# Optimization experiments

Hardware: AMD Instinct MI355X
Metric: run time of the kernel (lower is better)

Reference implementation:

```python
import jax, jax.numpy as jnp
import numpy as np

N = 100_000          # number of nodes
E = 3_200_000        # number of edges (avg degree 32)
IN_CH = 128
OUT_CH = 128


def setup_inputs() -> dict:
    key = jax.random.key(0)
    k1, k2, k3, k4 = jax.random.split(key, 4)
    x = jax.random.normal(k1, (N, IN_CH), dtype=jnp.float32)
    edge_index = jax.random.randint(k2, (2, E), 0, N, dtype=jnp.int32)
    # torch nn.Linear weights have shape [out_features, in_features]
    W_theta = jax.random.normal(k3, (OUT_CH, IN_CH), dtype=jnp.float32) / np.sqrt(IN_CH).astype(np.float32)
    W_phi = jax.random.normal(k4, (OUT_CH, OUT_CH), dtype=jnp.float32) / np.sqrt(OUT_CH).astype(np.float32)
    return {"x": x, "edge_index": edge_index, "W_theta": W_theta, "W_phi": W_phi}


def reference(x, edge_index, W_theta, W_phi):
    row, col = edge_index[0], edge_index[1]
    rel_pos = x[row] - x[col]                       # [E, in]
    rel_t = rel_pos @ W_theta.T                     # [E, out]
    aggr = jax.ops.segment_max(rel_t, row, num_segments=N)  # [N, out], -inf for empty segments
    # torch_scatter.scatter_max leaves empty segments at 0
    aggr = jnp.where(jnp.isneginf(aggr), jnp.zeros((), dtype=aggr.dtype), aggr)
    return aggr @ W_phi.T                           # [N, out]
```

## Files before the change

kernel.cpp:

```cpp
#include <hip/hip_runtime.h>
#include <stdint.h>

#define N_NODES 100000
#define N_EDGES 3200000
#define CH 128
#define NBUK 391
#define CAP 8704
#define SPLITB 391
#define EPB 8192
#define ROWS_A 50048

typedef __bf16 bf16x8 __attribute__((ext_vector_type(8)));
typedef float  floatx4 __attribute__((ext_vector_type(4)));

__device__ __forceinline__ unsigned short f2bf_bits(float f) {
    unsigned u = __float_as_uint(f);
    u += 0x7FFFu + ((u >> 16) & 1u);
    return (unsigned short)(u >> 16);
}

__device__ __forceinline__ unsigned short enc16(unsigned short b) {
    return b ^ ((b & 0x8000u) ? 0xFFFFu : 0x8000u);
}

__device__ __forceinline__ unsigned pkminu(unsigned a, unsigned b) {
    unsigned d;
    asm("v_pk_min_u16 %0, %1, %2" : "=v"(d) : "v"(a), "v"(b));
    return d;
}

__device__ __forceinline__ unsigned dec2(unsigned k) {
    unsigned lo = k & 0xFFFFu;
    unsigned hi = k >> 16;
    lo ^= (lo & 0x8000u) ? 0x8000u : 0xFFFFu;
    hi ^= (hi & 0x8000u) ? 0x8000u : 0xFFFFu;
    return lo | (hi << 16);
}

__device__ __forceinline__ bf16x8 pack8(floatx4 f0, floatx4 f1) {
    bf16x8 r;
    r[0] = (__bf16)f0[0]; r[1] = (__bf16)f0[1]; r[2] = (__bf16)f0[2]; r[3] = (__bf16)f0[3];
    r[4] = (__bf16)f1[0]; r[5] = (__bf16)f1[1]; r[6] = (__bf16)f1[2]; r[7] = (__bf16)f1[3];
    return r;
}

__device__ __forceinline__ void gemm_tile(int row0, int lane, const float* __restrict__ x,
                                          const unsigned short* __restrict__ wb,
                                          unsigned short* __restrict__ yt) {
    int m = lane & 15, quad = lane >> 4;
    bf16x8 a[4];
    const floatx4* xp = (const floatx4*)(x + (size_t)(row0 + m) * CH + quad * 8);
#pragma unroll
    for (int ks = 0; ks < 4; ks++) a[ks] = pack8(xp[ks * 8], xp[ks * 8 + 1]);

    for (int nt = 0; nt < 8; nt++) {
        const bf16x8* wp = (const bf16x8*)(wb + (size_t)(nt * 16 + m) * CH + quad * 8);
        floatx4 acc = {0.f, 0.f, 0.f, 0.f};
#pragma unroll
        for (int ks = 0; ks < 4; ks++)
            acc = __builtin_amdgcn_mfma_f32_16x16x32_bf16(a[ks], wp[ks * 4], acc, 0, 0, 0);
#pragma unroll
        for (int r = 0; r < 4; r++) {
            int orow = row0 + quad * 4 + r;
            yt[(size_t)orow * CH + nt * 16 + m] = enc16(f2bf_bits(acc[r]));
        }
    }
}

__global__ void k_setup(const float* __restrict__ Wt, const float* __restrict__ Wp,
                        unsigned short* __restrict__ wb, int* __restrict__ cursor) {
    int bid = blockIdx.x, t = threadIdx.x;
    if (bid < 128) {
        int i = bid * 256 + t;
        float v = (i < 16384) ? Wt[i] : Wp[i - 16384];
        wb[i] = f2bf_bits(v);
    } else {
        for (int i = t; i < NBUK; i += 256) cursor[i] = i * CAP;
    }
}

__global__ void k_split_gemmyA(const int* __restrict__ row, const int* __restrict__ col,
                               int* __restrict__ cursor, unsigned* __restrict__ pairs,
                               const float* __restrict__ x,
                               const unsigned short* __restrict__ wb,
                               unsigned short* __restrict__ yt) {
    __shared__ unsigned lpair[EPB];
    __shared__ int h[NBUK];
    __shared__ int hb[NBUK];
    __shared__ int lbase[NBUK];
    __shared__ int cur[NBUK];
    __shared__ int sc[512];
    int bid = blockIdx.x, t = threadIdx.x;
    if (bid < SPLITB) {
        for (int i = t; i < NBUK; i += 256) h[i] = 0;
        __syncthreads();
        int e0 = bid * EPB;
        int4 r[8];
        bool v[8];
#pragma unroll
        for (int j = 0; j < 8; j++) {
            int idx = e0 + j * 1024 + t * 4;
            v[j] = idx < N_EDGES;
            if (v[j]) {
                r[j] = *(const int4*)(row + idx);
                atomicAdd(&h[r[j].x >> 8], 1);
                atomicAdd(&h[r[j].y >> 8], 1);
                atomicAdd(&h[r[j].z >> 8], 1);
                atomicAdd(&h[r[j].w >> 8], 1);
            }
        }
        __syncthreads();
        for (int i = t; i < NBUK; i += 256) {
            int c = h[i];
            hb[i] = c ? atomicAdd(&cursor[i], c) : 0;
        }
        sc[t] = h[t];
        sc[t + 256] = (t + 256 < NBUK) ? h[t + 256] : 0;
        __syncthreads();
        for (int off = 1; off < 512; off <<= 1) {
            int a0 = (t >= off) ? sc[t - off] : 0;
            int a1 = (t + 256 >= off) ? sc[t + 256 - off] : 0;
            __syncthreads();
            sc[t] += a0;
            sc[t + 256] += a1;
            __syncthreads();
        }
        for (int i = t; i < NBUK; i += 256) {
            int lb = sc[i] - h[i];
            lbase[i] = lb;
            cur[i] = lb;
        }
        __syncthreads();
#pragma unroll
        for (int j = 0; j < 8; j++) {
            if (v[j]) {
                int idx = e0 + j * 1024 + t * 4;
                int4 c = *(const int4*)(col + idx);
                int b, p;
                b = r[j].x >> 8; p = atomicAdd(&cur[b], 1);
                lpair[p] = ((unsigned)(r[j].x & 255) << 17) | (unsigned)c.x;
                b = r[j].y >> 8; p = atomicAdd(&cur[b], 1);
                lpair[p] = ((unsigned)(r[j].y & 255) << 17) | (unsigned)c.y;
                b = r[j].z >> 8; p = atomicAdd(&cur[b], 1);
                lpair[p] = ((unsigned)(r[j].z & 255) << 17) | (unsigned)c.z;
                b = r[j].w >> 8; p = atomicAdd(&cur[b], 1);
                lpair[p] = ((unsigned)(r[j].w & 255) << 17) | (unsigned)c.w;
            }
        }
        __syncthreads();
        for (int b = t; b < NBUK; b += 256) {
            int n = h[b];
            if (!n) continue;
            int src = lbase[b];
            int dst = hb[b];
            int lim = (b + 1) * CAP - dst;
            if (n > lim) n = lim;
            for (int k = 0; k < n; k++) pairs[dst + k] = lpair[src + k];
        }
    } else {
        int wave = (bid - SPLITB) * 4 + (t >> 6);
        int row0 = wave * 16;
        if (row0 >= ROWS_A) return;
        gemm_tile(row0, t & 63, x, wb, yt);
    }
}

__global__ void k_build_gemmyB(unsigned* __restrict__ pairs, const int* __restrict__ cursor,
                               int* __restrict__ deg, int* __restrict__ offs,
                               const float* __restrict__ x,
                               const unsigned short* __restrict__ wb,
                               unsigned short* __restrict__ yt) {
    __shared__ int hist[256];
    __shared__ int sc[256];
    __shared__ int cur[256];
    __shared__ int lcsr[CAP];
    int bid = blockIdx.x, t = threadIdx.x;
    if (bid < NBUK) {
        int b = bid;
        int s0 = b * CAP;
        int cnt = cursor[b] - s0;
        if (cnt > CAP) cnt = CAP;
        if (t < 256) hist[t] = 0;
        __syncthreads();
        for (int i = t; i < cnt; i += 1024) {
            unsigned p = pairs[s0 + i];
            atomicAdd(&hist[p >> 17], 1);
        }
        __syncthreads();
        int d = 0;
        if (t < 256) { d = hist[t]; sc[t] = d; }
        __syncthreads();
        for (int off = 1; off < 256; off <<= 1) {
            int vv = 0;
            if (t < 256 && t >= off) vv = sc[t - off];
            __syncthreads();
            if (t < 256) sc[t] += vv;
            __syncthreads();
        }
        if (t < 256) {
            int excl = sc[t] - d;
            int node = b * 256 + t;
            if (node < N_NODES) {
                deg[node] = d;
                offs[node] = s0 + excl;
            }
            cur[t] = excl;
        }
        __syncthreads();
        for (int i = t; i < cnt; i += 1024) {
            unsigned p = pairs[s0 + i];
            int pos = atomicAdd(&cur[p >> 17], 1);
            lcsr[pos] = (int)(p & 0x1FFFFu);
        }
        __syncthreads();
        int* csr = (int*)pairs;
        for (int i = t; i < cnt; i += 1024) csr[s0 + i] = lcsr[i];
    } else {
        int wg = (bid - NBUK) * 16 + (t >> 6);
        int row0 = ROWS_A + wg * 16;
        if (row0 >= N_NODES) return;
        gemm_tile(row0, t & 63, x, wb, yt);
    }
}

#define PKA(v)                        \
    do {                              \
        m0 = pkminu(m0, (v).x);       \
        m1 = pkminu(m1, (v).y);       \
        m2 = pkminu(m2, (v).z);       \
        m3 = pkminu(m3, (v).w);       \
    } while (0)

__global__ void k_minaggr_out(const uint4* __restrict__ yt, const int* __restrict__ offs,
                              const int* __restrict__ deg, const int* __restrict__ csr,
                              const unsigned short* __restrict__ wb,
                              float* __restrict__ out) {
    __shared__ unsigned short atile[16 * 136];
    int t = threadIdx.x;
    int wave = t >> 6, lane = t & 63;
    int q = lane >> 4, s = lane & 15;
    int nl = wave * 4 + q;
    int n = blockIdx.x * 16 + nl;

    int i = offs[n];
    int len = deg[n];
    int end = i + len;

    unsigned m0 = ~0u, m1 = ~0u, m2 = ~0u, m3 = ~0u;

    for (; i + 8 <= end; i += 8) {
        int c0 = csr[i + 0];
        int c1 = csr[i + 1];
        int c2 = csr[i + 2];
        int c3 = csr[i + 3];
        int c4 = csr[i + 4];
        int c5 = csr[i + 5];
        int c6 = csr[i + 6];
        int c7 = csr[i + 7];
        uint4 v0 = yt[(size_t)c0 * 16 + s];
        uint4 v1 = yt[(size_t)c1 * 16 + s];
        uint4 v2 = yt[(size_t)c2 * 16 + s];
        uint4 v3 = yt[(size_t)c3 * 16 + s];
        uint4 v4 = yt[(size_t)c4 * 16 + s];
        uint4 v5 = yt[(size_t)c5 * 16 + s];
        uint4 v6 = yt[(size_t)c6 * 16 + s];
        uint4 v7 = yt[(size_t)c7 * 16 + s];
        PKA(v0); PKA(v1); PKA(v2); PKA(v3);
        PKA(v4); PKA(v5); PKA(v6); PKA(v7);
    }
    for (; i < end; i++) {
        int c = csr[i];
        uint4 v = yt[(size_t)c * 16 + s];
        PKA(v);
    }

    uint4 outv = {0u, 0u, 0u, 0u};
    if (len > 0) {
        unsigned d0 = dec2(m0), d1 = dec2(m1), d2 = dec2(m2), d3 = dec2(m3);
        uint4 se = yt[(size_t)n * 16 + s];
        unsigned s0 = dec2(se.x), s1 = dec2(se.y), s2 = dec2(se.z), s3 = dec2(se.w);
        outv.x = (unsigned)f2bf_bits(__uint_as_float(s0 << 16) - __uint_as_float(d0 << 16)) |
                 ((unsigned)f2bf_bits(__uint_as_float(s0 & 0xFFFF0000u) -
                                      __uint_as_float(d0 & 0xFFFF0000u)) << 16);
        outv.y = (unsigned)f2bf_bits(__uint_as_float(s1 << 16) - __uint_as_float(d1 << 16)) |
                 ((unsigned)f2bf_bits(__uint_as_float(s1 & 0xFFFF0000u) -
                                      __uint_as_float(d1 & 0xFFFF0000u)) << 16);
        outv.z = (unsigned)f2bf_bits(__uint_as_float(s2 << 16) - __uint_as_float(d2 << 16)) |
                 ((unsigned)f2bf_bits(__uint_as_float(s2 & 0xFFFF0000u) -
                                      __uint_as_float(d2 & 0xFFFF0000u)) << 16);
        outv.w = (unsigned)f2bf_bits(__uint_as_float(s3 << 16) - __uint_as_float(d3 << 16)) |
                 ((unsigned)f2bf_bits(__uint_as_float(s3 & 0xFFFF0000u) -
                                      __uint_as_float(d3 & 0xFFFF0000u)) << 16);
    }
    *(uint4*)&atile[nl * 136 + s * 8] = outv;
    __syncthreads();

    int m = lane & 15, quad = lane >> 4;
    bf16x8 a[4];
#pragma unroll
    for (int ks = 0; ks < 4; ks++)
        a[ks] = *(const bf16x8*)&atile[m * 136 + ks * 32 + quad * 8];

#pragma unroll
    for (int ntl = 0; ntl < 2; ntl++) {
        int nt = wave * 2 + ntl;
        const bf16x8* wp = (const bf16x8*)(wb + (size_t)(nt * 16 + m) * CH + quad * 8);
        floatx4 acc = {0.f, 0.f, 0.f, 0.f};
#pragma unroll
        for (int ks = 0; ks < 4; ks++)
            acc = __builtin_amdgcn_mfma_f32_16x16x32_bf16(a[ks], wp[ks * 4], acc, 0, 0, 0);
#pragma unroll
        for (int r = 0; r < 4; r++)
            out[(size_t)(blockIdx.x * 16 + quad * 4 + r) * CH + nt * 16 + m] = acc[r];
    }
}

extern "C" void kernel_launch(void* const* d_in, const int* in_sizes, int n_in,
                              void* d_out, int out_size, void* d_ws, size_t ws_size,
                              hipStream_t stream) {
    const float* x   = (const float*)d_in[0];
    const int* edge  = (const int*)d_in[1];
    const float* Wt  = (const float*)d_in[2];
    const float* Wp  = (const float*)d_in[3];
    const int* row = edge;
    const int* col = edge + N_EDGES;
    float* out = (float*)d_out;

    char* ws = (char*)d_ws;
    int* deg    = (int*)ws;  ws += 400128;
    int* offs   = (int*)ws;  ws += 400128;
    int* cursor = (int*)ws;  ws += 2048;
    unsigned short* yt = (unsigned short*)ws; ws += 25600000;
    unsigned short* wb = (unsigned short*)ws; ws += 65536;
    unsigned* pairs = (unsigned*)ws; ws += (size_t)NBUK * CAP * 4;

    k_setup<<<129, 256, 0, stream>>>(Wt, Wp, wb, cursor);
    k_split_gemmyA<<<SPLITB + 782, 256, 0, stream>>>(row, col, cursor, pairs, x, wb, yt);
    k_build_gemmyB<<<NBUK + 196, 1024, 0, stream>>>(pairs, cursor, deg, offs, x, wb, yt);
    k_minaggr_out<<<N_NODES / 16, 256, 0, stream>>>((const uint4*)yt, offs, deg,
                                                    (const int*)pairs, wb + 16384, out);
}
```

Baseline: 278.2 us.

## Fuse CSR build into min-aggregation kernel and move all node GEMM to split kernel

Removes the separate build kernel. Each bucket is now processed by two 512-thread blocks, one per half of the bucket's 256 nodes. Each block re-reads the bucket's pairs, builds a local CSR in shared memory, runs the packed-min gather over yt, and performs the output GEMM for its 128 nodes. The first-stage GEMM for all nodes moves into the split kernel, which drops one launch and the global CSR, deg and offs round trips. The cost is that every bucket's pairs are read twice, fewer and larger blocks run the gather, and each block holds more shared memory, which may reduce occupancy and latency hiding.

```diff
diff --git a/kernel.cpp b/kernel.cpp
--- a/kernel.cpp
+++ b/kernel.cpp
@@ -8,7 +8,6 @@
 #define CAP 8704
 #define SPLITB 391
 #define EPB 8192
-#define ROWS_A 50048
 
 typedef __bf16 bf16x8 __attribute__((ext_vector_type(8)));
 typedef float  floatx4 __attribute__((ext_vector_type(4)));
@@ -42,6 +41,26 @@
     r[0] = (__bf16)f0[0]; r[1] = (__bf16)f0[1]; r[2] = (__bf16)f0[2]; r[3] = (__bf16)f0[3];
     r[4] = (__bf16)f1[0]; r[5] = (__bf16)f1[1]; r[6] = (__bf16)f1[2]; r[7] = (__bf16)f1[3];
     return r;
+}
+
+__device__ __forceinline__ uint4 finish_half(unsigned m0, unsigned m1, unsigned m2, unsigned m3,
+                                             uint4 se) {
+    unsigned d0 = dec2(m0), d1 = dec2(m1), d2 = dec2(m2), d3 = dec2(m3);
+    unsigned s0 = dec2(se.x), s1 = dec2(se.y), s2 = dec2(se.z), s3 = dec2(se.w);
+    uint4 o;
+    o.x = (unsigned)f2bf_bits(__uint_as_float(s0 << 16) - __uint_as_float(d0 << 16)) |
+          ((unsigned)f2bf_bits(__uint_as_float(s0 & 0xFFFF0000u) -
+                               __uint_as_float(d0 & 0xFFFF0000u)) << 16);
+    o.y = (unsigned)f2bf_bits(__uint_as_float(s1 << 16) - __uint_as_float(d1 << 16)) |
+          ((unsigned)f2bf_bits(__uint_as_float(s1 & 0xFFFF0000u) -
+                               __uint_as_float(d1 & 0xFFFF0000u)) << 16);
+    o.z = (unsigned)f2bf_bits(__uint_as_float(s2 << 16) - __uint_as_float(d2 << 16)) |
+          ((unsigned)f2bf_bits(__uint_as_float(s2 & 0xFFFF0000u) -
+                               __uint_as_float(d2 & 0xFFFF0000u)) << 16);
+    o.w = (unsigned)f2bf_bits(__uint_as_float(s3 << 16) - __uint_as_float(d3 << 16)) |
+          ((unsigned)f2bf_bits(__uint_as_float(s3 & 0xFFFF0000u) -
+                               __uint_as_float(d3 & 0xFFFF0000u)) << 16);
+    return o;
 }
 
 __device__ __forceinline__ void gemm_tile(int row0, int lane, const float* __restrict__ x,
@@ -79,7 +98,7 @@
     }
 }
 
-__global__ void k_split_gemmyA(const int* __restrict__ row, const int* __restrict__ col,
+__global__ void k_split_gemmyF(const int* __restrict__ row, const int* __restrict__ col,
                                int* __restrict__ cursor, unsigned* __restrict__ pairs,
                                const float* __restrict__ x,
                                const unsigned short* __restrict__ wb,
@@ -160,158 +179,132 @@
     } else {
         int wave = (bid - SPLITB) * 4 + (t >> 6);
         int row0 = wave * 16;
-        if (row0 >= ROWS_A) return;
-        gemm_tile(row0, t & 63, x, wb, yt);
-    }
-}
-
-__global__ void k_build_gemmyB(unsigned* __restrict__ pairs, const int* __restrict__ cursor,
-                               int* __restrict__ deg, int* __restrict__ offs,
-                               const float* __restrict__ x,
-                               const unsigned short* __restrict__ wb,
-                               unsigned short* __restrict__ yt) {
-    __shared__ int hist[256];
-    __shared__ int sc[256];
-    __shared__ int cur[256];
-    __shared__ int lcsr[CAP];
-    int bid = blockIdx.x, t = threadIdx.x;
-    if (bid < NBUK) {
-        int b = bid;
-        int s0 = b * CAP;
-        int cnt = cursor[b] - s0;
-        if (cnt > CAP) cnt = CAP;
-        if (t < 256) hist[t] = 0;
-        __syncthreads();
-        for (int i = t; i < cnt; i += 1024) {
-            unsigned p = pairs[s0 + i];
-            atomicAdd(&hist[p >> 17], 1);
-        }
-        __syncthreads();
-        int d = 0;
-        if (t < 256) { d = hist[t]; sc[t] = d; }
-        __syncthreads();
-        for (int off = 1; off < 256; off <<= 1) {
-            int vv = 0;
-            if (t < 256 && t >= off) vv = sc[t - off];
-            __syncthreads();
-            if (t < 256) sc[t] += vv;
-            __syncthreads();
-        }
-        if (t < 256) {
-            int excl = sc[t] - d;
-            int node = b * 256 + t;
-            if (node < N_NODES) {
-                deg[node] = d;
-                offs[node] = s0 + excl;
-            }
-            cur[t] = excl;
-        }
-        __syncthreads();
-        for (int i = t; i < cnt; i += 1024) {
-            unsigned p = pairs[s0 + i];
-            int pos = atomicAdd(&cur[p >> 17], 1);
-            lcsr[pos] = (int)(p & 0x1FFFFu);
-        }
-        __syncthreads();
-        int* csr = (int*)pairs;
-        for (int i = t; i < cnt; i += 1024) csr[s0 + i] = lcsr[i];
-    } else {
-        int wg = (bid - NBUK) * 16 + (t >> 6);
-        int row0 = ROWS_A + wg * 16;
         if (row0 >= N_NODES) return;
         gemm_tile(row0, t & 63, x, wb, yt);
     }
 }
 
-#define PKA(v)                        \
+#define PK4(M, v)                     \
     do {                              \
-        m0 = pkminu(m0, (v).x);       \
-        m1 = pkminu(m1, (v).y);       \
-        m2 = pkminu(m2, (v).z);       \
-        m3 = pkminu(m3, (v).w);       \
+        (M).x = pkminu((M).x, (v).x); \
+        (M).y = pkminu((M).y, (v).y); \
+        (M).z = pkminu((M).z, (v).z); \
+        (M).w = pkminu((M).w, (v).w); \
     } while (0)
 
-__global__ void k_minaggr_out(const uint4* __restrict__ yt, const int* __restrict__ offs,
-                              const int* __restrict__ deg, const int* __restrict__ csr,
-                              const unsigned short* __restrict__ wb,
-                              float* __restrict__ out) {
-    __shared__ unsigned short atile[16 * 136];
+__global__ __launch_bounds__(512) void k_buildmin_out(
+        const unsigned* __restrict__ pairs, const int* __restrict__ cursor,
+        const uint4* __restrict__ yt, const unsigned short* __restrict__ wb,
+        float* __restrict__ out) {
+    __shared__ int hist[128];
+    __shared__ int scn[128];
+    __shared__ int basep[128];
+    __shared__ int curn[128];
+    __shared__ char ubuf[CAP * 4];
+    int* lcsr = (int*)ubuf;
+    unsigned short* atile = (unsigned short*)ubuf;
+
     int t = threadIdx.x;
+    int b = blockIdx.x >> 1;
+    int half = blockIdx.x & 1;
+    int s0 = b * CAP;
+    int cnt = cursor[b] - s0;
+    if (cnt > CAP) cnt = CAP;
+
+    if (t < 128) hist[t] = 0;
+    __syncthreads();
+    for (int i = t; i < cnt; i += 512) {
+        unsigned p = pairs[s0 + i];
+        int local = (int)(p >> 17);
+        if ((local >> 7) == half) atomicAdd(&hist[local & 127], 1);
+    }
+    __syncthreads();
+    int d = 0;
+    if (t < 128) { d = hist[t]; scn[t] = d; }
+    __syncthreads();
+    for (int off = 1; off < 128; off <<= 1) {
+        int vv = 0;
+        if (t < 128 && t >= off) vv = scn[t - off];
+        __syncthreads();
+        if (t < 128) scn[t] += vv;
+        __syncthreads();
+    }
+    if (t < 128) {
+        int excl = scn[t] - d;
+        basep[t] = excl;
+        curn[t] = excl;
+    }
+    __syncthreads();
+    for (int i = t; i < cnt; i += 512) {
+        unsigned p = pairs[s0 + i];
+        int local = (int)(p >> 17);
+        if ((local >> 7) == half) {
+            int pos = atomicAdd(&curn[local & 127], 1);
+            lcsr[pos] = (int)(p & 0x1FFFFu);
+        }
+    }
+    __syncthreads();
+
+    int s16 = t & 15;
+    int nsub = t >> 4;
+    uint4 sv[4];
+#pragma unroll
+    for (int ng = 0; ng < 4; ng++) {
+        int l = ng * 32 + nsub;
+        int i = basep[l];
+        int len = hist[l];
+        int end = i + len;
+        uint4 M = {~0u, ~0u, ~0u, ~0u};
+        for (; i + 8 <= end; i += 8) {
+            int c0 = lcsr[i + 0], c1 = lcsr[i + 1], c2 = lcsr[i + 2], c3 = lcsr[i + 3];
+            int c4 = lcsr[i + 4], c5 = lcsr[i + 5], c6 = lcsr[i + 6], c7 = lcsr[i + 7];
+            uint4 v0 = yt[(size_t)c0 * 16 + s16];
+            uint4 v1 = yt[(size_t)c1 * 16 + s16];
+            uint4 v2 = yt[(size_t)c2 * 16 + s16];
+            uint4 v3 = yt[(size_t)c3 * 16 + s16];
+            uint4 v4 = yt[(size_t)c4 * 16 + s16];
+            uint4 v5 = yt[(size_t)c5 * 16 + s16];
+            uint4 v6 = yt[(size_t)c6 * 16 + s16];
+            uint4 v7 = yt[(size_t)c7 * 16 + s16];
+            PK4(M, v0); PK4(M, v1); PK4(M, v2); PK4(M, v3);
+            PK4(M, v4); PK4(M, v5); PK4(M, v6); PK4(M, v7);
+        }
+        for (; i < end; i++) {
+            uint4 v = yt[(size_t)lcsr[i] * 16 + s16];
+            PK4(M, v);
+        }
+        uint4 outv = {0u, 0u, 0u, 0u};
+        if (len > 0) {
+            int n = blockIdx.x * 128 + l;
+            outv = finish_half(M.x, M.y, M.z, M.w, yt[(size_t)n * 16 + s16]);
+        }
+        sv[ng] = outv;
+    }
+    __syncthreads();
+#pragma unroll
+    for (int ng = 0; ng < 4; ng++)
+        *(uint4*)&atile[(ng * 32 + nsub) * 136 + s16 * 8] = sv[ng];
+    __syncthreads();
+
     int wave = t >> 6, lane = t & 63;
-    int q = lane >> 4, s = lane & 15;
-    int nl = wave * 4 + q;
-    int n = blockIdx.x * 16 + nl;
-
-    int i = offs[n];
-    int len = deg[n];
-    int end = i + len;
-
-    unsigned m0 = ~0u, m1 = ~0u, m2 = ~0u, m3 = ~0u;
-
-    for (; i + 8 <= end; i += 8) {
-        int c0 = csr[i + 0];
-        int c1 = csr[i + 1];
-        int c2 = csr[i + 2];
-        int c3 = csr[i + 3];
-        int c4 = csr[i + 4];
-        int c5 = csr[i + 5];
-        int c6 = csr[i + 6];
-        int c7 = csr[i + 7];
-        uint4 v0 = yt[(size_t)c0 * 16 + s];
-        uint4 v1 = yt[(size_t)c1 * 16 + s];
-        uint4 v2 = yt[(size_t)c2 * 16 + s];
-        uint4 v3 = yt[(size_t)c3 * 16 + s];
-        uint4 v4 = yt[(size_t)c4 * 16 + s];
-        uint4 v5 = yt[(size_t)c5 * 16 + s];
-        uint4 v6 = yt[(size_t)c6 * 16 + s];
-        uint4 v7 = yt[(size_t)c7 * 16 + s];
-        PKA(v0); PKA(v1); PKA(v2); PKA(v3);
-        PKA(v4); PKA(v5); PKA(v6); PKA(v7);
-    }
-    for (; i < end; i++) {
-        int c = csr[i];
-        uint4 v = yt[(size_t)c * 16 + s];
-        PKA(v);
-    }
-
-    uint4 outv = {0u, 0u, 0u, 0u};
-    if (len > 0) {
-        unsigned d0 = dec2(m0), d1 = dec2(m1), d2 = dec2(m2), d3 = dec2(m3);
-        uint4 se = yt[(size_t)n * 16 + s];
-        unsigned s0 = dec2(se.x), s1 = dec2(se.y), s2 = dec2(se.z), s3 = dec2(se.w);
-        outv.x = (unsigned)f2bf_bits(__uint_as_float(s0 << 16) - __uint_as_float(d0 << 16)) |
-                 ((unsigned)f2bf_bits(__uint_as_float(s0 & 0xFFFF0000u) -
-                                      __uint_as_float(d0 & 0xFFFF0000u)) << 16);
-        outv.y = (unsigned)f2bf_bits(__uint_as_float(s1 << 16) - __uint_as_float(d1 << 16)) |
-                 ((unsigned)f2bf_bits(__uint_as_float(s1 & 0xFFFF0000u) -
-                                      __uint_as_float(d1 & 0xFFFF0000u)) << 16);
-        outv.z = (unsigned)f2bf_bits(__uint_as_float(s2 << 16) - __uint_as_float(d2 << 16)) |
-                 ((unsigned)f2bf_bits(__uint_as_float(s2 & 0xFFFF0000u) -
-                                      __uint_as_float(d2 & 0xFFFF0000u)) << 16);
-        outv.w = (unsigned)f2bf_bits(__uint_as_float(s3 << 16) - __uint_as_float(d3 << 16)) |
-                 ((unsigned)f2bf_bits(__uint_as_float(s3 & 0xFFFF0000u) -
-                                      __uint_as_float(d3 & 0xFFFF0000u)) << 16);
-    }
-    *(uint4*)&atile[nl * 136 + s * 8] = outv;
-    __syncthreads();
-
     int m = lane & 15, quad = lane >> 4;
     bf16x8 a[4];
 #pragma unroll
     for (int ks = 0; ks < 4; ks++)
-        a[ks] = *(const bf16x8*)&atile[m * 136 + ks * 32 + quad * 8];
-
-#pragma unroll
-    for (int ntl = 0; ntl < 2; ntl++) {
-        int nt = wave * 2 + ntl;
+        a[ks] = *(const bf16x8*)&atile[(wave * 16 + m) * 136 + ks * 32 + quad * 8];
+
+    for (int nt = 0; nt < 8; nt++) {
         const bf16x8* wp = (const bf16x8*)(wb + (size_t)(nt * 16 + m) * CH + quad * 8);
         floatx4 acc = {0.f, 0.f, 0.f, 0.f};
 #pragma unroll
         for (int ks = 0; ks < 4; ks++)
             acc = __builtin_amdgcn_mfma_f32_16x16x32_bf16(a[ks], wp[ks * 4], acc, 0, 0, 0);
 #pragma unroll
-        for (int r = 0; r < 4; r++)
-            out[(size_t)(blockIdx.x * 16 + quad * 4 + r) * CH + nt * 16 + m] = acc[r];
+        for (int r = 0; r < 4; r++) {
+            int orow = blockIdx.x * 128 + wave * 16 + quad * 4 + r;
+            if (orow < N_NODES)
+                out[(size_t)orow * CH + nt * 16 + m] = acc[r];
+        }
     }
 }
 
@@ -327,16 +320,13 @@
     float* out = (float*)d_out;
 
     char* ws = (char*)d_ws;
-    int* deg    = (int*)ws;  ws += 400128;
-    int* offs   = (int*)ws;  ws += 400128;
     int* cursor = (int*)ws;  ws += 2048;
     unsigned short* yt = (unsigned short*)ws; ws += 25600000;
     unsigned short* wb = (unsigned short*)ws; ws += 65536;
     unsigned* pairs = (unsigned*)ws; ws += (size_t)NBUK * CAP * 4;
 
     k_setup<<<129, 256, 0, stream>>>(Wt, Wp, wb, cursor);
-    k_split_gemmyA<<<SPLITB + 782, 256, 0, stream>>>(row, col, cursor, pairs, x, wb, yt);
-    k_build_gemmyB<<<NBUK + 196, 1024, 0, stream>>>(pairs, cursor, deg, offs, x, wb, yt);
-    k_minaggr_out<<<N_NODES / 16, 256, 0, stream>>>((const uint4*)yt, offs, deg,
-                                                    (const int*)pairs, wb + 16384, out);
-}
+    k_split_gemmyF<<<SPLITB + 1563, 256, 0, stream>>>(row, col, cursor, pairs, x, wb, yt);
+    k_buildmin_out<<<2 * NBUK, 512, 0, stream>>>(pairs, cursor, (const uint4*)yt,
+                                                 wb + 16384, out);
+}
```

After: 292.8 us. +5.2%, slower.
